# Performance work log

Hardware: AMD Instinct MI355X
Metric: run time of the kernel (lower is better)

The kernel has to match this reference:

```python
import jax, jax.numpy as jnp
import numpy as np

B, HP, WP = 4, 32, 32
T = HP * WP
C = 768            # n_embd
NH = 24            # n_head
HS = C // NH       # head_size == HEAD_SIZE == 32
E = HS             # TIME_MIX_EXTRA_DIM = HEAD_SIZE
D = 64             # TIME_DECAY_DIM


def setup_inputs() -> dict:
    key = jax.random.key(0)
    ks = jax.random.split(key, 24)
    small = lambda k, sh: jax.random.uniform(k, sh, jnp.float32, -1e-4, 1e-4)
    inp = {
        "x": jax.random.normal(ks[0], (B, T, C), jnp.float32),
        "time_maa_x": jax.random.uniform(ks[1], (1, 1, C), jnp.float32),
        "time_maa_w": jax.random.uniform(ks[2], (1, 1, C), jnp.float32),
        "time_maa_k": jax.random.uniform(ks[3], (1, 1, C), jnp.float32),
        "time_maa_v": jax.random.uniform(ks[4], (1, 1, C), jnp.float32),
        "time_maa_r": jax.random.uniform(ks[5], (1, 1, C), jnp.float32),
        "time_maa_g": jax.random.uniform(ks[6], (1, 1, C), jnp.float32),
        "time_maa_w1": small(ks[7], (C, 5 * E)),
        "time_maa_w2": small(ks[8], (5, E, C)),
        "time_decay": jnp.linspace(-6.0, -1.0, C, dtype=jnp.float32).reshape(1, 1, C),
        "time_decay_w1": small(ks[9], (C, D)),
        "time_decay_w2": small(ks[10], (D, C)),
        "time_faaaa": jax.random.uniform(ks[11], (NH, HS), jnp.float32, -0.1, 0.6),
        "W_r": jax.random.normal(ks[12], (C, C), jnp.float32) * 0.02,
        "W_k": jax.random.normal(ks[13], (C, C), jnp.float32) * 0.02,
        "W_v": jax.random.normal(ks[14], (C, C), jnp.float32) * 0.02,
        "W_g": jax.random.normal(ks[15], (C, C), jnp.float32) * 0.02,
        "W_o": jax.random.normal(ks[16], (C, C), jnp.float32) * 0.02,
        "ln_w": jnp.ones((C,), jnp.float32),
        "ln_b": jnp.zeros((C,), jnp.float32),
        "Hp": HP,
        "Wp": WP,
    }
    return inp


def q_shift(x, H, W):
    """groups_q_shift with K=1, gamma=1/4: quarter-channel 4-direction spatial shift, zero-padded."""
    Bs, Ts, Cs = x.shape
    g = x.reshape(Bs, H, W, Cs)
    c4 = Cs // 4
    a, b, c, d = g[..., :c4], g[..., c4:2 * c4], g[..., 2 * c4:3 * c4], g[..., 3 * c4:]
    a = jnp.pad(a[:, :, :-1], ((0, 0), (0, 0), (1, 0), (0, 0)))  # shift +W (right)
    b = jnp.pad(b[:, :, 1:], ((0, 0), (0, 0), (0, 1), (0, 0)))   # shift -W (left)
    c = jnp.pad(c[:, :-1], ((0, 0), (1, 0), (0, 0), (0, 0)))     # shift +H (down)
    d = jnp.pad(d[:, 1:], ((0, 0), (0, 1), (0, 0), (0, 0)))      # shift -H (up)
    return jnp.concatenate([a, b, c, d], axis=-1).reshape(Bs, Ts, Cs)


def wkv6(r, k, v, w, u):
    """RWKV6 WKV scan. r,k,v,w: (B,T,C); u: (NH,HS). decay = exp(-exp(w))."""
    Bs, Ts, Cs = r.shape
    rh = r.reshape(Bs, Ts, NH, HS)
    kh = k.reshape(Bs, Ts, NH, HS)
    vh = v.reshape(Bs, Ts, NH, HS)
    dh = jnp.exp(-jnp.exp(w)).reshape(Bs, Ts, NH, HS)

    def step(s, ins):
        rt, kt, vt, dt = ins                                   # each (B,NH,HS)
        kv = kt[..., :, None] * vt[..., None, :]               # (B,NH,HS,HS)
        y = jnp.einsum('bhj,bhji->bhi', rt, s + u[None, :, :, None] * kv)
        s = dt[..., :, None] * s + kv
        return s, y

    xs = (rh.transpose(1, 0, 2, 3), kh.transpose(1, 0, 2, 3),
          vh.transpose(1, 0, 2, 3), dh.transpose(1, 0, 2, 3))
    s0 = jnp.zeros((Bs, NH, HS, HS), r.dtype)
    _, ys = jax.lax.scan(step, s0, xs)                          # (T,B,NH,HS)
    return ys.transpose(1, 0, 2, 3).reshape(Bs, Ts, Cs)


def reference(x, time_maa_x, time_maa_w, time_maa_k, time_maa_v, time_maa_r,
              time_maa_g, time_maa_w1, time_maa_w2, time_decay, time_decay_w1,
              time_decay_w2, time_faaaa, W_r, W_k, W_v, W_g, W_o, ln_w, ln_b,
              Hp, Wp):
    Bs, Ts, Cs = x.shape
    xx = q_shift(x, Hp, Wp) - x                                 # token shift delta
    xxx = x + xx * time_maa_x
    xxx = jnp.tanh(xxx @ time_maa_w1).reshape(Bs, Ts, 5, E)
    mix = jnp.einsum('btke,kec->kbtc', xxx, time_maa_w2)        # (5,B,T,C)
    mw, mk, mv, mr, mg = mix[0], mix[1], mix[2], mix[3], mix[4]

    xw = x + xx * (time_maa_w + mw)
    xk = x + xx * (time_maa_k + mk)
    xv = x + xx * (time_maa_v + mv)
    xr = x + xx * (time_maa_r + mr)
    xg = x + xx * (time_maa_g + mg)

    r = xr @ W_r
    k = xk @ W_k
    v = xv @ W_v
    g = jax.nn.silu(xg @ W_g)

    ww = jnp.tanh(xw @ time_decay_w1) @ time_decay_w2
    w = time_decay + ww                                         # data-dependent log-decay

    y = wkv6(r, k, v, w, time_faaaa)

    # ln_x (LayerNorm over channels)
    mu = y.mean(-1, keepdims=True)
    var = ((y - mu) ** 2).mean(-1, keepdims=True)
    yn = (y - mu) / jnp.sqrt(var + 1e-5) * ln_w + ln_b

    return (yn * g) @ W_o
```

## Files before the change

kernel.cpp:

```cpp
#include <hip/hip_runtime.h>
#include <math.h>

#define BB   4
#define TT   1024
#define CC   768
#define NH_  24
#define HS_  32
#define NBH  (BB * NH_)
#define NCH  16
#define CL   64

static constexpr size_t SZ = (size_t)BB * TT * CC;

typedef __attribute__((ext_vector_type(8))) __bf16 bf16x8;
typedef __attribute__((ext_vector_type(4))) float  f32x4;

__device__ __forceinline__ unsigned short f2bf(float f) {
    unsigned u = __float_as_uint(f);
    unsigned r = (u + 0x7FFFu + ((u >> 16) & 1u)) >> 16;
    return (unsigned short)r;
}
__device__ __forceinline__ float bf2f(unsigned short h) {
    return __uint_as_float(((unsigned)h) << 16);
}

struct TDesc { const float* src; unsigned short* dst; int R, C; };
struct TArgs { TDesc d[8]; };

__global__ __launch_bounds__(256) void transpose_cast(TArgs a)
{
    __shared__ float tile[32][33];
    TDesc t = a.d[blockIdx.z];
    const int tx0 = blockIdx.x * 32, ty0 = blockIdx.y * 32;
    if (tx0 >= t.C || ty0 >= t.R) return;
    const int tx = threadIdx.x & 31, ty = threadIdx.x >> 5;
    #pragma unroll
    for (int dy = 0; dy < 4; ++dy) {
        int rr = ty0 + ty + dy * 8, cc = tx0 + tx;
        tile[ty + dy * 8][tx] = (rr < t.R && cc < t.C) ? t.src[(size_t)rr * t.C + cc] : 0.f;
    }
    __syncthreads();
    #pragma unroll
    for (int dy = 0; dy < 4; ++dy) {
        int cc = tx0 + ty + dy * 8, rr = ty0 + tx;
        if (cc < t.C && rr < t.R)
            t.dst[(size_t)cc * t.R + rr] = f2bf(tile[tx][ty + dy * 8]);
    }
}

__global__ __launch_bounds__(192) void w2fill(const float* __restrict__ w2,
                                              unsigned short* __restrict__ W2t)
{
    const int n = blockIdx.x;
    const int e = threadIdx.x;
    if (e >= 160) return;
    const int kk = n / 768;
    const int c  = n - kk * 768;
    unsigned short val = 0;
    if ((e >> 5) == kk) val = f2bf(w2[(size_t)e * 768 + c]);
    W2t[(size_t)n * 160 + e] = val;
}

__global__ __launch_bounds__(256) void shift_kernel(
    const float* __restrict__ x, const float* __restrict__ maa_x,
    float* __restrict__ xxO, unsigned short* __restrict__ xxxO)
{
    const int tok = blockIdx.x;
    const int t   = tok & (TT - 1);
    const int hh  = t >> 5;
    const int wp  = t & 31;
    const int tid = threadIdx.x;
    const float* xrow = x + (size_t)tok * CC;
    for (int c = tid; c < CC; c += 256) {
        float xc = xrow[c];
        float sh;
        if (c < 192)      sh = (wp > 0)  ? xrow[c - CC]      : 0.f;
        else if (c < 384) sh = (wp < 31) ? xrow[c + CC]      : 0.f;
        else if (c < 576) sh = (hh > 0)  ? xrow[c - 32 * CC] : 0.f;
        else              sh = (hh < 31) ? xrow[c + 32 * CC] : 0.f;
        float xxv = sh - xc;
        size_t o = (size_t)tok * CC + c;
        xxO[o]  = xxv;
        xxxO[o] = f2bf(fmaf(xxv, maa_x[c], xc));
    }
}

template<int KDIM, class Epi>
__device__ __forceinline__ void gemm_core(const unsigned short* __restrict__ A,
                                          const unsigned short* __restrict__ W,
                                          int N, const Epi& epi)
{
    __shared__ __align__(16) unsigned short As[64][40];
    __shared__ __align__(16) unsigned short Bs[64][40];

    const int tid  = threadIdx.x;
    const int lane = tid & 63;
    const int wv   = tid >> 6;
    const int wm   = (wv >> 1) * 32, wn = (wv & 1) * 32;
    const int m0   = blockIdx.y * 64, n0 = blockIdx.x * 64;
    const int srow = tid >> 2, scb = (tid & 3) * 8;
    const int l15  = lane & 15, kb8 = (lane >> 4) * 8;

    f32x4 acc[2][2];
    #pragma unroll
    for (int a = 0; a < 2; ++a)
        #pragma unroll
        for (int b = 0; b < 2; ++b)
            #pragma unroll
            for (int e = 0; e < 4; ++e) acc[a][b][e] = 0.f;

    const unsigned short* aP = A + (size_t)(m0 + srow) * KDIM + scb;
    const unsigned short* bP = W + (size_t)(n0 + srow) * KDIM + scb;
    const bool bvalid = (n0 + srow) < N;

    for (int k0 = 0; k0 < KDIM; k0 += 32) {
        uint4 av = *(const uint4*)(aP + k0);
        uint4 bw = make_uint4(0u, 0u, 0u, 0u);
        if (bvalid) bw = *(const uint4*)(bP + k0);
        *(uint4*)&As[srow][scb] = av;
        *(uint4*)&Bs[srow][scb] = bw;
        __syncthreads();

        bf16x8 a0 = *(const bf16x8*)&As[wm + l15][kb8];
        bf16x8 a1 = *(const bf16x8*)&As[wm + 16 + l15][kb8];
        bf16x8 b0 = *(const bf16x8*)&Bs[wn + l15][kb8];
        bf16x8 b1 = *(const bf16x8*)&Bs[wn + 16 + l15][kb8];
        acc[0][0] = __builtin_amdgcn_mfma_f32_16x16x32_bf16(a0, b0, acc[0][0], 0, 0, 0);
        acc[0][1] = __builtin_amdgcn_mfma_f32_16x16x32_bf16(a0, b1, acc[0][1], 0, 0, 0);
        acc[1][0] = __builtin_amdgcn_mfma_f32_16x16x32_bf16(a1, b0, acc[1][0], 0, 0, 0);
        acc[1][1] = __builtin_amdgcn_mfma_f32_16x16x32_bf16(a1, b1, acc[1][1], 0, 0, 0);
        __syncthreads();
    }

    const int rb_ = m0 + wm + (lane >> 4) * 4;
    #pragma unroll
    for (int mi = 0; mi < 2; ++mi)
        #pragma unroll
        for (int ni = 0; ni < 2; ++ni) {
            int col = n0 + wn + ni * 16 + l15;
            if (col < N) {
                #pragma unroll
                for (int j = 0; j < 4; ++j)
                    epi(rb_ + mi * 16 + j, col, acc[mi][ni][j]);
            }
        }
}

template<int KDIM, class Epi>
__device__ __forceinline__ void gemm_core128(const unsigned short* __restrict__ A,
                                             const unsigned short* __restrict__ W,
                                             int N, const Epi& epi)
{
    __shared__ __align__(16) unsigned short As[128][40];
    __shared__ __align__(16) unsigned short Bs[128][40];

    const int tid  = threadIdx.x;
    const int lane = tid & 63;
    const int wv   = tid >> 6;
    const int wm   = (wv >> 1) * 64, wn = (wv & 1) * 64;
    const int m0   = blockIdx.y * 128, n0 = blockIdx.x * 128;
    const int l15  = lane & 15, kb8 = (lane >> 4) * 8, rb4 = (lane >> 4) * 4;
    const int sr   = tid >> 2, sq = (tid & 3) * 8;

    f32x4 acc[4][4];
    #pragma unroll
    for (int a = 0; a < 4; ++a)
        #pragma unroll
        for (int b = 0; b < 4; ++b)
            #pragma unroll
            for (int e = 0; e < 4; ++e) acc[a][b][e] = 0.f;

    const unsigned short* aP  = A + (size_t)(m0 + sr) * KDIM + sq;
    const unsigned short* aP2 = aP + (size_t)64 * KDIM;
    const unsigned short* bP  = W + (size_t)(n0 + sr) * KDIM + sq;
    const unsigned short* bP2 = bP + (size_t)64 * KDIM;
    const bool bv1 = (n0 + sr) < N, bv2 = (n0 + 64 + sr) < N;

    for (int k0 = 0; k0 < KDIM; k0 += 32) {
        uint4 a1 = *(const uint4*)(aP + k0);
        uint4 a2 = *(const uint4*)(aP2 + k0);
        uint4 b1 = make_uint4(0u, 0u, 0u, 0u);
        uint4 b2 = make_uint4(0u, 0u, 0u, 0u);
        if (bv1) b1 = *(const uint4*)(bP + k0);
        if (bv2) b2 = *(const uint4*)(bP2 + k0);
        *(uint4*)&As[sr][sq]      = a1;
        *(uint4*)&As[64 + sr][sq] = a2;
        *(uint4*)&Bs[sr][sq]      = b1;
        *(uint4*)&Bs[64 + sr][sq] = b2;
        __syncthreads();

        bf16x8 af[4], bfr[4];
        #pragma unroll
        for (int mi = 0; mi < 4; ++mi)
            af[mi] = *(const bf16x8*)&As[wm + mi * 16 + l15][kb8];
        #pragma unroll
        for (int ni = 0; ni < 4; ++ni)
            bfr[ni] = *(const bf16x8*)&Bs[wn + ni * 16 + l15][kb8];
        #pragma unroll
        for (int mi = 0; mi < 4; ++mi)
            #pragma unroll
            for (int ni = 0; ni < 4; ++ni)
                acc[mi][ni] = __builtin_amdgcn_mfma_f32_16x16x32_bf16(af[mi], bfr[ni], acc[mi][ni], 0, 0, 0);
        __syncthreads();
    }

    const int rbase = m0 + wm + rb4;
    #pragma unroll
    for (int mi = 0; mi < 4; ++mi)
        #pragma unroll
        for (int ni = 0; ni < 4; ++ni) {
            int col = n0 + wn + ni * 16 + l15;
            if (col < N) {
                #pragma unroll
                for (int j = 0; j < 4; ++j)
                    epi(rbase + mi * 16 + j, col, acc[mi][ni][j]);
            }
        }
}

struct EpiTanh {
    unsigned short* O; int ldo;
    __device__ void operator()(int r, int c, float v) const {
        O[(size_t)r * ldo + c] = f2bf(tanhf(v));
    }
};
struct EpiF32 {
    float* O;
    __device__ void operator()(int r, int c, float v) const {
        O[(size_t)r * 768 + c] = v;
    }
};
struct EpiDec {
    const float* td; float* O;
    __device__ void operator()(int r, int c, float v) const {
        O[(size_t)r * 768 + c] = expf(-expf(td[c] + v));
    }
};
struct EpiMix {
    const float* px; const float* pxx;
    const float* maa[5];
    unsigned short* outs[5];
    __device__ void operator()(int r, int c, float v) const {
        int kk = c / 768;
        int cc = c - kk * 768;
        size_t o = (size_t)r * 768 + cc;
        outs[kk][o] = f2bf(fmaf(pxx[o], maa[kk][cc] + v, px[o]));
    }
};
struct EpiRKVG {
    unsigned short* O; bool silu;
    __device__ void operator()(int r, int c, float v) const {
        if (silu) v = v / (1.f + expf(-v));
        O[(size_t)r * 768 + c] = f2bf(v);
    }
};

template<int KDIM, class Epi>
__global__ __launch_bounds__(256) void gemm_one(const unsigned short* __restrict__ A,
                                                const unsigned short* __restrict__ W,
                                                int N, Epi epi)
{
    gemm_core<KDIM>(A, W, N, epi);
}

template<int KDIM, class Epi>
__global__ __launch_bounds__(256) void gemm_one128(const unsigned short* __restrict__ A,
                                                   const unsigned short* __restrict__ W,
                                                   int N, Epi epi)
{
    gemm_core128<KDIM>(A, W, N, epi);
}

struct QuadArgs {
    const unsigned short* A[4];
    const unsigned short* W[4];
    unsigned short* O[4];
};
__global__ __launch_bounds__(256) void gemm_quad768(QuadArgs q)
{
    const int z = blockIdx.z;
    EpiRKVG e{q.O[z], z == 3};
    gemm_core128<768>(q.A[z], q.W[z], 768, e);
}

__global__ __launch_bounds__(256) void wkv_local(
    const unsigned short* __restrict__ r, const unsigned short* __restrict__ k,
    const unsigned short* __restrict__ v, const float* __restrict__ dec,
    const float* __restrict__ u, float* __restrict__ y,
    unsigned short* __restrict__ rsb, float* __restrict__ kvt,
    float* __restrict__ dcv)
{
    __shared__ __align__(16) unsigned short rwL[64][40], kwL[64][40];
    __shared__ __align__(16) unsigned short vT0[32][40], vT1[32][40];
    __shared__ __align__(16) unsigned short ksT0[32][40], ksT1[32][40];
    __shared__ __align__(16) unsigned short PL0[64][40], PL1[64][40];
    __shared__ float AL[65][32];
    __shared__ float segprod[8][32];
    __shared__ float dpart[64][4];
    __shared__ float diagL[64];
    __shared__ float uL[32];

    const int c   = blockIdx.x;
    const int bh  = blockIdx.y;
    const int b = bh / NH_, h = bh % NH_;
    const int tid  = threadIdx.x;
    const int lane = tid & 63;
    const int wv   = tid >> 6;
    const int l15  = lane & 15;
    const int kb8  = (lane >> 4) * 8;
    const int rb4  = (lane >> 4) * 4;
    const int tc   = c * CL;

    const size_t base0 = ((size_t)b * TT) * CC + (size_t)h * HS_;

    if (tid < 32) uL[tid] = u[h * HS_ + tid];

    const int lrow = tid >> 2, lq = (tid & 3) * 8;
    const int cj = tid & 31, cseg = tid >> 5;

    {
        size_t gp = base0 + (size_t)(tc + lrow) * CC + lq;
        uint4 rv = *(const uint4*)(r + gp);
        uint4 kv = *(const uint4*)(k + gp);
        uint4 vv = *(const uint4*)(v + gp);
        *(uint4*)&rwL[lrow][lq] = rv;
        *(uint4*)&kwL[lrow][lq] = kv;
        const unsigned short* vp = (const unsigned short*)&vv;
        if (lrow < 32) {
            #pragma unroll
            for (int e = 0; e < 8; ++e) vT0[lq + e][lrow] = vp[e];
        } else {
            #pragma unroll
            for (int e = 0; e < 8; ++e) vT1[lq + e][lrow - 32] = vp[e];
        }
    }
    float dv[8];
    #pragma unroll
    for (int q = 0; q < 8; ++q)
        dv[q] = dec[base0 + (size_t)(tc + cseg * 8 + q) * CC + cj];
    {
        float lp = dv[0];
        #pragma unroll
        for (int q = 1; q < 8; ++q) lp *= dv[q];
        segprod[cseg][cj] = lp;
    }
    __syncthreads();

    {
        const int ptau = tid >> 2, pp = tid & 3;
        float acc = 0.f;
        #pragma unroll
        for (int e = 0; e < 8; ++e) {
            int j = pp * 8 + e;
            acc += bf2f(rwL[ptau][j]) * uL[j] * bf2f(kwL[ptau][j]);
        }
        dpart[ptau][pp] = acc;
    }
    {
        float pre = 1.f;
        #pragma unroll
        for (int s = 0; s < 7; ++s) if (s < cseg) pre *= segprod[s][cj];
        float run = pre;
        #pragma unroll
        for (int q = 0; q < 8; ++q) {
            AL[cseg * 8 + q][cj] = run;
            run *= dv[q];
        }
        if (cseg == 7) AL[64][cj] = run;
    }
    __syncthreads();

    if (tid < 64)
        diagL[tid] = dpart[tid][0] + dpart[tid][1] + dpart[tid][2] + dpart[tid][3];
    if (tid < 32)
        dcv[((size_t)bh * NCH + c) * 32 + tid] = AL[64][tid];

    #pragma unroll
    for (int q = 0; q < 8; ++q) {
        int tau = cseg * 8 + q;
        float a  = AL[tau][cj];
        float ia = 1.f / AL[tau + 1][cj];
        unsigned short rs = f2bf(bf2f(rwL[tau][cj]) * a);
        unsigned short ks = f2bf(bf2f(kwL[tau][cj]) * ia);
        rwL[tau][cj] = rs;
        kwL[tau][cj] = ks;
        if (tau < 32) ksT0[cj][tau] = ks; else ksT1[cj][tau - 32] = ks;
    }
    __syncthreads();

    {
        const int wm = (wv >> 1) * 32, wn = (wv & 1) * 32;
        bf16x8 a0 = *(const bf16x8*)&rwL[wm + l15][kb8];
        bf16x8 a1 = *(const bf16x8*)&rwL[wm + 16 + l15][kb8];
        bf16x8 b0 = *(const bf16x8*)&kwL[wn + l15][kb8];
        bf16x8 b1 = *(const bf16x8*)&kwL[wn + 16 + l15][kb8];
        f32x4 qf[2][2];
        #pragma unroll
        for (int mi = 0; mi < 2; ++mi)
            #pragma unroll
            for (int ni = 0; ni < 2; ++ni)
                #pragma unroll
                for (int e = 0; e < 4; ++e) qf[mi][ni][e] = 0.f;
        qf[0][0] = __builtin_amdgcn_mfma_f32_16x16x32_bf16(a0, b0, qf[0][0], 0, 0, 0);
        qf[0][1] = __builtin_amdgcn_mfma_f32_16x16x32_bf16(a0, b1, qf[0][1], 0, 0, 0);
        qf[1][0] = __builtin_amdgcn_mfma_f32_16x16x32_bf16(a1, b0, qf[1][0], 0, 0, 0);
        qf[1][1] = __builtin_amdgcn_mfma_f32_16x16x32_bf16(a1, b1, qf[1][1], 0, 0, 0);
        #pragma unroll
        for (int mi = 0; mi < 2; ++mi)
            #pragma unroll
            for (int ni = 0; ni < 2; ++ni) {
                const int col = wn + ni * 16 + l15;
                #pragma unroll
                for (int jj = 0; jj < 4; ++jj) {
                    const int row = wm + mi * 16 + rb4 + jj;
                    float val = (col < row) ? qf[mi][ni][jj]
                              : ((col == row) ? diagL[row] : 0.f);
                    unsigned short bvv = f2bf(val);
                    if (col < 32) PL0[row][col] = bvv;
                    else          PL1[row][col - 32] = bvv;
                }
            }
    }
    __syncthreads();

    *(uint4*)(rsb + base0 + (size_t)(tc + lrow) * CC + lq) = *(const uint4*)&rwL[lrow][lq];

    {
        const int mr = wv * 16;
        bf16x8 pa0 = *(const bf16x8*)&PL0[mr + l15][kb8];
        bf16x8 pa1 = *(const bf16x8*)&PL1[mr + l15][kb8];
        #pragma unroll
        for (int ni = 0; ni < 2; ++ni) {
            bf16x8 bv0 = *(const bf16x8*)&vT0[ni * 16 + l15][kb8];
            bf16x8 bv1 = *(const bf16x8*)&vT1[ni * 16 + l15][kb8];
            f32x4 acc;
            #pragma unroll
            for (int e = 0; e < 4; ++e) acc[e] = 0.f;
            acc = __builtin_amdgcn_mfma_f32_16x16x32_bf16(pa0, bv0, acc, 0, 0, 0);
            acc = __builtin_amdgcn_mfma_f32_16x16x32_bf16(pa1, bv1, acc, 0, 0, 0);
            #pragma unroll
            for (int jj = 0; jj < 4; ++jj)
                y[base0 + (size_t)(tc + mr + rb4 + jj) * CC + ni * 16 + l15] = acc[jj];
        }
    }

    {
        const int mi_ = (wv >> 1) * 16, nj = (wv & 1) * 16;
        bf16x8 av0 = *(const bf16x8*)&vT0[mi_ + l15][kb8];
        bf16x8 av1 = *(const bf16x8*)&vT1[mi_ + l15][kb8];
        bf16x8 bk0 = *(const bf16x8*)&ksT0[nj + l15][kb8];
        bf16x8 bk1 = *(const bf16x8*)&ksT1[nj + l15][kb8];
        f32x4 acc;
        #pragma unroll
        for (int e = 0; e < 4; ++e) acc[e] = 0.f;
        acc = __builtin_amdgcn_mfma_f32_16x16x32_bf16(av0, bk0, acc, 0, 0, 0);
        acc = __builtin_amdgcn_mfma_f32_16x16x32_bf16(av1, bk1, acc, 0, 0, 0);
        const int j = nj + l15;
        const size_t sb = ((size_t)bh * NCH + c) << 10;
        #pragma unroll
        for (int jj = 0; jj < 4; ++jj)
            kvt[sb + (size_t)(mi_ + rb4 + jj) * 32 + j] = acc[jj];
    }
}

__global__ __launch_bounds__(256) void wkv_carry(
    const float* __restrict__ kvt, const float* __restrict__ dcv,
    unsigned short* __restrict__ spv)
{
    const int bh = blockIdx.x;
    const int tid = threadIdx.x;
    const int e0 = tid << 2;
    const int j0 = e0 & 31;
    float s0 = 0.f, s1 = 0.f, s2 = 0.f, s3 = 0.f;
    #pragma unroll
    for (int c = 0; c < NCH; ++c) {
        const size_t sb = (size_t)bh * NCH + c;
        float4 kv = *(const float4*)(kvt + (sb << 10) + e0);
        float4 d4 = *(const float4*)(dcv + sb * 32 + j0);
        s0 = d4.x * (s0 + kv.x);
        s1 = d4.y * (s1 + kv.y);
        s2 = d4.z * (s2 + kv.z);
        s3 = d4.w * (s3 + kv.w);
        if (c < NCH - 1) {
            unsigned lo = (unsigned)f2bf(s0) | ((unsigned)f2bf(s1) << 16);
            unsigned hi = (unsigned)f2bf(s2) | ((unsigned)f2bf(s3) << 16);
            *(uint2*)(spv + ((sb + 1) << 10) + e0) = make_uint2(lo, hi);
        }
    }
}

__global__ __launch_bounds__(256) void wkv_stadd(
    const unsigned short* __restrict__ rsb, const unsigned short* __restrict__ spv,
    float* __restrict__ y)
{
    __shared__ __align__(16) unsigned short rsL[64][40];
    __shared__ __align__(16) unsigned short STb[32][40];

    const int c  = blockIdx.x + 1;
    const int bh = blockIdx.y;
    const int b = bh / NH_, h = bh % NH_;
    const int tid = threadIdx.x, lane = tid & 63, wv = tid >> 6;
    const int l15 = lane & 15, kb8 = (lane >> 4) * 8, rb4 = (lane >> 4) * 4;
    const int tc = c * CL;
    const size_t base0 = ((size_t)b * TT) * CC + (size_t)h * HS_;
    const int lrow = tid >> 2, lq = (tid & 3) * 8;

    *(uint4*)&rsL[lrow][lq] = *(const uint4*)(rsb + base0 + (size_t)(tc + lrow) * CC + lq);
    if (tid < 128) {
        int row = tid >> 2, q = (tid & 3) * 8;
        *(uint4*)&STb[row][q] =
            *(const uint4*)(spv + (((size_t)bh * NCH + c) << 10) + (size_t)row * 32 + q);
    }
    __syncthreads();

    const int mr = wv * 16;
    bf16x8 ra = *(const bf16x8*)&rsL[mr + l15][kb8];
    #pragma unroll
    for (int ni = 0; ni < 2; ++ni) {
        bf16x8 bs = *(const bf16x8*)&STb[ni * 16 + l15][kb8];
        f32x4 acc;
        #pragma unroll
        for (int e = 0; e < 4; ++e) acc[e] = 0.f;
        acc = __builtin_amdgcn_mfma_f32_16x16x32_bf16(ra, bs, acc, 0, 0, 0);
        #pragma unroll
        for (int jj = 0; jj < 4; ++jj) {
            size_t gp = base0 + (size_t)(tc + mr + rb4 + jj) * CC + ni * 16 + l15;
            y[gp] += acc[jj];
        }
    }
}

__global__ __launch_bounds__(256) void ln_gate(
    const float* __restrict__ y, const unsigned short* __restrict__ g,
    const float* __restrict__ lnw, const float* __restrict__ lnb,
    unsigned short* __restrict__ z)
{
    __shared__ float sy[CC];
    __shared__ float rbuf[8];
    __shared__ float stats[2];

    const int row = blockIdx.x, tid = threadIdx.x;
    const float* yr = y + (size_t)row * CC;

    float s1 = 0.f, s2 = 0.f;
    #pragma unroll
    for (int q = 0; q < 3; ++q) {
        int c = tid + q * 256;
        float vv = yr[c];
        sy[c] = vv;
        s1 += vv;
        s2 += vv * vv;
    }
    #pragma unroll
    for (int off = 32; off > 0; off >>= 1) {
        s1 += __shfl_down(s1, off);
        s2 += __shfl_down(s2, off);
    }
    const int wid = tid >> 6;
    if ((tid & 63) == 0) { rbuf[wid] = s1; rbuf[4 + wid] = s2; }
    __syncthreads();
    if (tid == 0) {
        float S1 = rbuf[0] + rbuf[1] + rbuf[2] + rbuf[3];
        float S2 = rbuf[4] + rbuf[5] + rbuf[6] + rbuf[7];
        float mu = S1 / (float)CC;
        float var = S2 / (float)CC - mu * mu;
        stats[0] = mu;
        stats[1] = rsqrtf(var + 1e-5f);
    }
    __syncthreads();
    const float mu = stats[0], rstd = stats[1];
    const unsigned short* gr = g + (size_t)row * CC;
    unsigned short* zr = z + (size_t)row * CC;
    #pragma unroll
    for (int q = 0; q < 3; ++q) {
        int c = tid + q * 256;
        zr[c] = f2bf(fmaf((sy[c] - mu) * rstd, lnw[c], lnb[c]) * bf2f(gr[c]));
    }
}

extern "C" void kernel_launch(void* const* d_in, const int* in_sizes, int n_in,
                              void* d_out, int out_size, void* d_ws, size_t ws_size,
                              hipStream_t stream)
{
    const float* x      = (const float*)d_in[0];
    const float* maa_x  = (const float*)d_in[1];
    const float* maa_w  = (const float*)d_in[2];
    const float* maa_k  = (const float*)d_in[3];
    const float* maa_v  = (const float*)d_in[4];
    const float* maa_r  = (const float*)d_in[5];
    const float* maa_g  = (const float*)d_in[6];
    const float* w1     = (const float*)d_in[7];
    const float* w2     = (const float*)d_in[8];
    const float* tdec   = (const float*)d_in[9];
    const float* tdw1   = (const float*)d_in[10];
    const float* tdw2   = (const float*)d_in[11];
    const float* faaaa  = (const float*)d_in[12];
    const float* Wr     = (const float*)d_in[13];
    const float* Wk     = (const float*)d_in[14];
    const float* Wv     = (const float*)d_in[15];
    const float* Wg     = (const float*)d_in[16];
    const float* Wo     = (const float*)d_in[17];
    const float* lnw    = (const float*)d_in[18];
    const float* lnb    = (const float*)d_in[19];

    char* base = (char*)d_ws;
    size_t off = 0;
    auto alloc = [&](size_t bytes) -> char* {
        char* p = base + off;
        off = (off + bytes + 255) & ~(size_t)255;
        return p;
    };

    float*          xx   = (float*)alloc(SZ * 4);
    float*          decb = (float*)alloc(SZ * 4);
    unsigned short* xxx  = (unsigned short*)alloc(SZ * 2);
    unsigned short* xw   = (unsigned short*)alloc(SZ * 2);
    unsigned short* xk   = (unsigned short*)alloc(SZ * 2);
    unsigned short* xv   = (unsigned short*)alloc(SZ * 2);
    unsigned short* xr   = (unsigned short*)alloc(SZ * 2);
    unsigned short* xg   = (unsigned short*)alloc(SZ * 2);
    unsigned short* rb   = (unsigned short*)alloc(SZ * 2);
    unsigned short* kb   = (unsigned short*)alloc(SZ * 2);
    unsigned short* vb   = (unsigned short*)alloc(SZ * 2);
    unsigned short* gb   = (unsigned short*)alloc(SZ * 2);
    unsigned short* t5   = (unsigned short*)alloc((size_t)4096 * 160 * 2);
    unsigned short* d1   = (unsigned short*)alloc((size_t)4096 * 64 * 2);
    unsigned short* w1t  = (unsigned short*)alloc((size_t)160 * 768 * 2);
    unsigned short* w2t  = (unsigned short*)alloc((size_t)3840 * 160 * 2);
    unsigned short* wrt  = (unsigned short*)alloc((size_t)768 * 768 * 2);
    unsigned short* wkt  = (unsigned short*)alloc((size_t)768 * 768 * 2);
    unsigned short* wvt  = (unsigned short*)alloc((size_t)768 * 768 * 2);
    unsigned short* wgt  = (unsigned short*)alloc((size_t)768 * 768 * 2);
    unsigned short* wot  = (unsigned short*)alloc((size_t)768 * 768 * 2);
    unsigned short* td1t = (unsigned short*)alloc((size_t)64 * 768 * 2);
    unsigned short* td2t = (unsigned short*)alloc((size_t)768 * 64 * 2);

    float*          y    = xx;
    unsigned short* z    = xxx;
    unsigned short* rsb  = xr;
    float*          kvtb = (float*)xk;
    unsigned short* spvb = xv;
    float*          dcb  = (float*)xg;

    TArgs ta = {{
        { w1,   w1t,  768, 160 },
        { Wr,   wrt,  768, 768 },
        { Wk,   wkt,  768, 768 },
        { Wv,   wvt,  768, 768 },
        { Wg,   wgt,  768, 768 },
        { Wo,   wot,  768, 768 },
        { tdw1, td1t, 768, 64  },
        { tdw2, td2t, 64,  768 },
    }};
    transpose_cast<<<dim3(24, 24, 8), 256, 0, stream>>>(ta);
    w2fill<<<3840, 192, 0, stream>>>(w2, w2t);

    shift_kernel<<<BB * TT, 256, 0, stream>>>(x, maa_x, xx, xxx);

    gemm_one<768, EpiTanh><<<dim3(3, 64), 256, 0, stream>>>(xxx, w1t, 160, EpiTanh{t5, 160});

    EpiMix em{ x, xx,
               { maa_w, maa_k, maa_v, maa_r, maa_g },
               { xw, xk, xv, xr, xg } };
    gemm_one128<160, EpiMix><<<dim3(30, 32), 256, 0, stream>>>(t5, w2t, 3840, em);

    gemm_one<768, EpiTanh><<<dim3(1, 64), 256, 0, stream>>>(xw, td1t, 64, EpiTanh{d1, 64});

    gemm_one<64, EpiDec><<<dim3(12, 64), 256, 0, stream>>>(d1, td2t, 768, EpiDec{tdec, decb});

    QuadArgs qa = {{ xr, xk, xv, xg }, { wrt, wkt, wvt, wgt }, { rb, kb, vb, gb }};
    gemm_quad768<<<dim3(6, 32, 4), 256, 0, stream>>>(qa);

    wkv_local<<<dim3(NCH, NBH), 256, 0, stream>>>(rb, kb, vb, decb, faaaa, y, rsb, kvtb, dcb);
    wkv_carry<<<NBH, 256, 0, stream>>>(kvtb, dcb, spvb);
    wkv_stadd<<<dim3(NCH - 1, NBH), 256, 0, stream>>>(rsb, spvb, y);

    ln_gate<<<BB * TT, 256, 0, stream>>>(y, gb, lnw, lnb, z);

    gemm_one128<768, EpiF32><<<dim3(6, 32), 256, 0, stream>>>(z, wot, 768, EpiF32{(float*)d_out});
}
```

Before: 302.7 us.

## Use direct global-to-LDS loads and XCD-aware block swizzle in 128-tile GEMMs

```diff
diff --git a/kernel.cpp b/kernel.cpp
--- a/kernel.cpp
+++ b/kernel.cpp
@@ -22,6 +22,19 @@
 }
 __device__ __forceinline__ float bf2f(unsigned short h) {
     return __uint_as_float(((unsigned)h) << 16);
+}
+
+__device__ __forceinline__ void gload16(const unsigned short* g, unsigned short* l)
+{
+    __builtin_amdgcn_global_load_lds(
+        (const __attribute__((address_space(1))) void*)(g),
+        (__attribute__((address_space(3))) void*)(l),
+        16, 0, 0);
+}
+
+__device__ __forceinline__ int xcd_swz(int wg, int nwg)
+{
+    return (wg & 7) * (nwg >> 3) + (wg >> 3);
 }
 
 struct TDesc { const float* src; unsigned short* dst; int R, C; };
@@ -149,16 +162,15 @@
 template<int KDIM, class Epi>
 __device__ __forceinline__ void gemm_core128(const unsigned short* __restrict__ A,
                                              const unsigned short* __restrict__ W,
-                                             int N, const Epi& epi)
-{
-    __shared__ __align__(16) unsigned short As[128][40];
-    __shared__ __align__(16) unsigned short Bs[128][40];
+                                             int N, int m0, int n0, const Epi& epi)
+{
+    __shared__ __align__(16) unsigned short As[128][32];
+    __shared__ __align__(16) unsigned short Bs[128][32];
 
     const int tid  = threadIdx.x;
     const int lane = tid & 63;
     const int wv   = tid >> 6;
     const int wm   = (wv >> 1) * 64, wn = (wv & 1) * 64;
-    const int m0   = blockIdx.y * 128, n0 = blockIdx.x * 128;
     const int l15  = lane & 15, kb8 = (lane >> 4) * 8, rb4 = (lane >> 4) * 4;
     const int sr   = tid >> 2, sq = (tid & 3) * 8;
 
@@ -171,22 +183,19 @@
             for (int e = 0; e < 4; ++e) acc[a][b][e] = 0.f;
 
     const unsigned short* aP  = A + (size_t)(m0 + sr) * KDIM + sq;
-    const unsigned short* aP2 = aP + (size_t)64 * KDIM;
+    const unsigned short* aP2 = A + (size_t)(m0 + 64 + sr) * KDIM + sq;
     const unsigned short* bP  = W + (size_t)(n0 + sr) * KDIM + sq;
-    const unsigned short* bP2 = bP + (size_t)64 * KDIM;
-    const bool bv1 = (n0 + sr) < N, bv2 = (n0 + 64 + sr) < N;
+    const unsigned short* bP2 = W + (size_t)(n0 + 64 + sr) * KDIM + sq;
+    unsigned short* asD  = &As[sr][sq];
+    unsigned short* asD2 = &As[64 + sr][sq];
+    unsigned short* bsD  = &Bs[sr][sq];
+    unsigned short* bsD2 = &Bs[64 + sr][sq];
 
     for (int k0 = 0; k0 < KDIM; k0 += 32) {
-        uint4 a1 = *(const uint4*)(aP + k0);
-        uint4 a2 = *(const uint4*)(aP2 + k0);
-        uint4 b1 = make_uint4(0u, 0u, 0u, 0u);
-        uint4 b2 = make_uint4(0u, 0u, 0u, 0u);
-        if (bv1) b1 = *(const uint4*)(bP + k0);
-        if (bv2) b2 = *(const uint4*)(bP2 + k0);
-        *(uint4*)&As[sr][sq]      = a1;
-        *(uint4*)&As[64 + sr][sq] = a2;
-        *(uint4*)&Bs[sr][sq]      = b1;
-        *(uint4*)&Bs[64 + sr][sq] = b2;
+        gload16(aP + k0,  asD);
+        gload16(aP2 + k0, asD2);
+        gload16(bP + k0,  bsD);
+        gload16(bP2 + k0, bsD2);
         __syncthreads();
 
         bf16x8 af[4], bfr[4];
@@ -263,12 +272,14 @@
     gemm_core<KDIM>(A, W, N, epi);
 }
 
-template<int KDIM, class Epi>
+template<int KDIM, int NB, class Epi>
 __global__ __launch_bounds__(256) void gemm_one128(const unsigned short* __restrict__ A,
                                                    const unsigned short* __restrict__ W,
                                                    int N, Epi epi)
 {
-    gemm_core128<KDIM>(A, W, N, epi);
+    const int idx = xcd_swz(blockIdx.x, gridDim.x);
+    const int m0 = (idx / NB) * 128, n0 = (idx % NB) * 128;
+    gemm_core128<KDIM>(A, W, N, m0, n0, epi);
 }
 
 struct QuadArgs {
@@ -278,9 +289,12 @@
 };
 __global__ __launch_bounds__(256) void gemm_quad768(QuadArgs q)
 {
-    const int z = blockIdx.z;
+    const int idx = xcd_swz(blockIdx.x, 768);
+    const int z = idx / 192;
+    const int rz = idx - z * 192;
+    const int m0 = (rz / 6) * 128, n0 = (rz % 6) * 128;
     EpiRKVG e{q.O[z], z == 3};
-    gemm_core128<768>(q.A[z], q.W[z], 768, e);
+    gemm_core128<768>(q.A[z], q.W[z], 768, m0, n0, e);
 }
 
 __global__ __launch_bounds__(256) void wkv_local(
@@ -662,14 +676,14 @@
     EpiMix em{ x, xx,
                { maa_w, maa_k, maa_v, maa_r, maa_g },
                { xw, xk, xv, xr, xg } };
-    gemm_one128<160, EpiMix><<<dim3(30, 32), 256, 0, stream>>>(t5, w2t, 3840, em);
+    gemm_one128<160, 30, EpiMix><<<960, 256, 0, stream>>>(t5, w2t, 3840, em);
 
     gemm_one<768, EpiTanh><<<dim3(1, 64), 256, 0, stream>>>(xw, td1t, 64, EpiTanh{d1, 64});
 
     gemm_one<64, EpiDec><<<dim3(12, 64), 256, 0, stream>>>(d1, td2t, 768, EpiDec{tdec, decb});
 
     QuadArgs qa = {{ xr, xk, xv, xg }, { wrt, wkt, wvt, wgt }, { rb, kb, vb, gb }};
-    gemm_quad768<<<dim3(6, 32, 4), 256, 0, stream>>>(qa);
+    gemm_quad768<<<768, 256, 0, stream>>>(qa);
 
     wkv_local<<<dim3(NCH, NBH), 256, 0, stream>>>(rb, kb, vb, decb, faaaa, y, rsb, kvtb, dcb);
     wkv_carry<<<NBH, 256, 0, stream>>>(kvtb, dcb, spvb);
@@ -677,5 +691,5 @@
 
     ln_gate<<<BB * TT, 256, 0, stream>>>(y, gb, lnw, lnb, z);
 
-    gemm_one128<768, EpiF32><<<dim3(6, 32), 256, 0, stream>>>(z, wot, 768, EpiF32{(float*)d_out});
-}
+    gemm_one128<768, 6, EpiF32><<<192, 256, 0, stream>>>(z, wot, 768, EpiF32{(float*)d_out});
+}
```

New measurement: 267.2 us. 11.7% less time.
